# Performance work log

Measured on AMD Instinct MI355X. Metric: run time of the kernel, lower is better.

## Reference

```python
import jax, jax.numpy as jnp
import numpy as np
import math

D_MODEL = 1024
NUM_HEADS = 16
D_HEAD = D_MODEL // NUM_HEADS          # 64
N_FREQ = D_HEAD // 2 + 1               # 33 rfft bins
COMPRESSION_RATIO = 0.5


def setup_inputs() -> dict:
    key = jax.random.key(0)
    k_x, k_qkv, k_out, k_b, k_m = jax.random.split(key, 5)
    B, S = 2, 2048
    x = jax.random.normal(k_x, (B, S, D_MODEL), dtype=jnp.float32)
    # Linear weights stored as [in, out] (torch Linear uses [out, in]; math identical).
    w_qkv = jax.random.normal(k_qkv, (D_MODEL, 3 * D_MODEL), dtype=jnp.float32) / math.sqrt(D_MODEL)
    w_out = jax.random.normal(k_out, (D_MODEL, D_MODEL), dtype=jnp.float32) / math.sqrt(D_MODEL)
    b_out = jax.random.normal(k_b, (D_MODEL,), dtype=jnp.float32) * 0.01
    # Learned per-frequency-bin mask logits of AdaptiveFrequencyMask(d_state=d_head).
    # Initialized around logit(compression_ratio) with small noise.
    init_logit = math.log(COMPRESSION_RATIO / (1.0 - COMPRESSION_RATIO))
    mask_logits = init_logit + 0.1 * jax.random.normal(k_m, (N_FREQ,), dtype=jnp.float32)
    return {"x": x, "w_qkv": w_qkv, "w_out": w_out, "b_out": b_out, "mask_logits": mask_logits}


def _spectral_filter(t, mask):
    # rfft over d_head dim, apply learned soft mask, inverse rfft.  t: [B,H,S,dh]
    tf = jnp.fft.rfft(t, axis=-1)          # [B,H,S,N_FREQ] complex
    tf = tf * mask                          # broadcast real mask over bins
    return jnp.fft.irfft(tf, n=t.shape[-1], axis=-1).astype(t.dtype)


def reference(x, w_qkv, w_out, b_out, mask_logits):
    B, S, D = x.shape
    H, dh = NUM_HEADS, D_HEAD
    qkv = x @ w_qkv                                         # [B,S,3D]
    q, k, v = jnp.split(qkv, 3, axis=-1)
    # [B,S,D] -> [B,H,S,dh]
    to_heads = lambda t: t.reshape(B, S, H, dh).transpose(0, 2, 1, 3)
    q, k, v = to_heads(q), to_heads(k), to_heads(v)
    mask = jax.nn.sigmoid(mask_logits)                      # [N_FREQ]
    q = _spectral_filter(q, mask)
    k = _spectral_filter(k, mask)
    scores = jnp.einsum('bhqd,bhkd->bhqk', q, k) / math.sqrt(dh)
    attn = jax.nn.softmax(scores, axis=-1)                  # dropout p=0 (eval)
    out = jnp.einsum('bhqk,bhkd->bhqd', attn, v)
    out = out.transpose(0, 2, 1, 3).reshape(B, S, D)
    return out @ w_out + b_out
```

## Files before the change

### kernel.cpp

```cpp
#include <hip/hip_runtime.h>

#define S_LEN 2048
#define NH    16
#define DH    64
#define DM    1024
#define NQKV  3072

typedef __attribute__((ext_vector_type(8))) __bf16 bf16x8;
typedef __attribute__((ext_vector_type(4))) float  f32x4;
typedef unsigned short ushort_t;

static __device__ __forceinline__ unsigned short bf16b(float f) {
  return __builtin_bit_cast(unsigned short, (__bf16)f);
}

static __device__ __forceinline__ float exp2v(float x) {
  return __builtin_amdgcn_exp2f(x);
}

static __device__ __forceinline__ bf16x8 pack8(float4 f0, float4 f1) {
  uint4 v;
  v.x = ((unsigned)bf16b(f0.y) << 16) | bf16b(f0.x);
  v.y = ((unsigned)bf16b(f0.w) << 16) | bf16b(f0.z);
  v.z = ((unsigned)bf16b(f1.y) << 16) | bf16b(f1.x);
  v.w = ((unsigned)bf16b(f1.w) << 16) | bf16b(f1.z);
  return __builtin_bit_cast(bf16x8, v);
}

static __device__ __forceinline__ void glds16(const void* g, void* l) {
  __builtin_amdgcn_global_load_lds((const __attribute__((address_space(1))) unsigned int*)g,
                                   (__attribute__((address_space(3))) unsigned int*)l, 16, 0, 0);
}

#define OFF_WT  65536ull
#define OFF_WOT 6356992ull
#define OFF_Q   8454144ull
#define OFF_K   16842752ull
#define OFF_V   25231360ull
#define OFF_AO  33619968ull

__global__ __launch_bounds__(256) void k_prep(const float* __restrict__ wqkv,
                                              const float* __restrict__ wout,
                                              const float* __restrict__ x,
                                              const float* __restrict__ logits,
                                              unsigned short* __restrict__ Wt,
                                              unsigned short* __restrict__ Wot,
                                              unsigned short* __restrict__ xb) {
  __shared__ __align__(16) char sbuf[16640];
  int bid = blockIdx.x;
  int t = threadIdx.x;

  if (bid < 256) {
    float* msk = (float*)sbuf;
    float* Kd  = (float*)(sbuf + 144);
    ushort_t (*Fb)[72] = (ushort_t(*)[72])(sbuf + 416);
    if (t < 33) msk[t] = 1.0f / (1.0f + __expf(-logits[t]));
    __syncthreads();
    if (t < 64) {
      float acc = msk[0];
      #pragma unroll
      for (int f = 1; f < 32; ++f) {
        int r = (f * t) & 63;
        acc += 2.0f * msk[f] * __cosf((float)r * (6.28318530717958647692f / 64.0f));
      }
      acc += msk[32] * ((t & 1) ? -1.0f : 1.0f);
      Kd[t] = acc * (1.0f / 64.0f);
    }
    __syncthreads();
    for (int idx = t; idx < 4096; idx += 256) {
      int j = idx >> 6, i = idx & 63;
      Fb[j][i] = bf16b(Kd[(j - i) & 63]);
    }
    __syncthreads();

    int lane = t & 63, w = t >> 6;
    int m16 = lane & 15, quad = lane >> 4;
    int kx = bid >> 5, yy = bid & 31;
    int which = yy >> 4, h = yy & 15;
    int base = which * 1024 + h * 64;

    bf16x8 af0 = *(const bf16x8*)(&Fb[w * 16 + m16][quad * 8]);
    bf16x8 af1 = *(const bf16x8*)(&Fb[w * 16 + m16][32 + quad * 8]);

    f32x4 acc[8] = {};
    #pragma unroll 2
    for (int n = 0; n < 8; ++n) {
      const float* Wg = wqkv + (size_t)(kx * 128 + n * 16 + m16) * NQKV + base + quad * 8;
      float4 a0 = *(const float4*)(Wg);
      float4 a1 = *(const float4*)(Wg + 4);
      float4 b0 = *(const float4*)(Wg + 32);
      float4 b1 = *(const float4*)(Wg + 36);
      acc[n] = __builtin_amdgcn_mfma_f32_16x16x32_bf16(af0, pack8(a0, a1), acc[n], 0, 0, 0);
      acc[n] = __builtin_amdgcn_mfma_f32_16x16x32_bf16(af1, pack8(b0, b1), acc[n], 0, 0, 0);
    }
    float sc = (which == 0) ? 0.18033688011112042f : 1.0f;
    #pragma unroll
    for (int n = 0; n < 8; ++n) {
      #pragma unroll
      for (int r = 0; r < 4; ++r) {
        int j = w * 16 + quad * 4 + r;
        Wt[(size_t)(base + j) * DM + kx * 128 + n * 16 + m16] = bf16b(acc[n][r] * sc);
      }
    }
  } else if (bid < 768) {
    float (*Ts)[65] = (float(*)[65])sbuf;
    int b1 = bid - 256;
    if (b1 < 256) {
      int kt = b1 & 15, nt = b1 >> 4;
      int cb = 2048 + nt * 64, kbase = kt * 64;
      #pragma unroll
      for (int p = 0; p < 16; ++p) {
        int kk = p * 4 + (t >> 6);
        Ts[kk][t & 63] = wqkv[(size_t)(kbase + kk) * NQKV + cb + (t & 63)];
      }
      __syncthreads();
      #pragma unroll
      for (int p = 0; p < 16; ++p) {
        int nn = p * 4 + (t >> 6);
        Wt[(size_t)(cb + nn) * DM + kbase + (t & 63)] = bf16b(Ts[t & 63][nn]);
      }
    } else {
      int b2 = b1 - 256;
      int kt = b2 & 15, nt = b2 >> 4;
      int cb = nt * 64, kbase = kt * 64;
      #pragma unroll
      for (int p = 0; p < 16; ++p) {
        int kk = p * 4 + (t >> 6);
        Ts[kk][t & 63] = wout[(size_t)(kbase + kk) * DM + cb + (t & 63)];
      }
      __syncthreads();
      #pragma unroll
      for (int p = 0; p < 16; ++p) {
        int nn = p * 4 + (t >> 6);
        Wot[(size_t)(cb + nn) * DM + kbase + (t & 63)] = bf16b(Ts[t & 63][nn]);
      }
    }
  } else {
    size_t i = ((size_t)(bid - 768) * 256 + t) * 8;
    const float4* xp = (const float4*)(x + i);
    float4 a = xp[0], b = xp[1];
    uint4 v;
    v.x = ((unsigned)bf16b(a.y) << 16) | bf16b(a.x);
    v.y = ((unsigned)bf16b(a.w) << 16) | bf16b(a.z);
    v.z = ((unsigned)bf16b(b.y) << 16) | bf16b(b.x);
    v.w = ((unsigned)bf16b(b.w) << 16) | bf16b(b.z);
    *(uint4*)(xb + i) = v;
  }
}

template<int BM, int BN, int WCOLS, int MR, int NR>
__device__ __forceinline__ void gemm_core2(const unsigned short* __restrict__ A,
                                           const unsigned short* __restrict__ Bw,
                                           int bm, int bn, unsigned short* smem,
                                           f32x4 (&acc)[MR][NR]) {
  constexpr int SLOT = (BM + BN) * 64;
  constexpr int PA = BM / 64, PB = BN / 64;
  constexpr int L = PA + PB;
  int t = threadIdx.x, lane = t & 63, w = t >> 6;
  int m16 = lane & 15, quad = lane >> 4;
  int wr = (w / WCOLS) * (MR * 16), wc = (w % WCOLS) * (NR * 16);
  int xr = m16 & 7;
  int trow = t >> 3, tcol = t & 7;
  int gsw = (tcol ^ (trow & 7)) * 8;
  const unsigned short* Ag = A  + (size_t)(bm * BM + trow) * DM + gsw;
  const unsigned short* Bg = Bw + (size_t)(bn * BN + trow) * DM + gsw;
  unsigned short* Al = smem + trow * 64 + tcol * 8;
  unsigned short* Bl = smem + BM * 64 + trow * 64 + tcol * 8;

  #pragma unroll
  for (int s = 0; s < 2; ++s) {
    #pragma unroll
    for (int p = 0; p < PA; ++p)
      glds16(Ag + (size_t)p * 64 * DM + s * 64, Al + s * SLOT + p * 4096);
    #pragma unroll
    for (int p = 0; p < PB; ++p)
      glds16(Bg + (size_t)p * 64 * DM + s * 64, Bl + s * SLOT + p * 4096);
  }

  #pragma unroll 1
  for (int ks = 0; ks < 16; ++ks) {
    if (ks < 15) asm volatile("s_waitcnt vmcnt(%0)" :: "n"(L) : "memory");
    else         asm volatile("s_waitcnt vmcnt(0)" ::: "memory");
    __builtin_amdgcn_s_barrier();
    __builtin_amdgcn_sched_barrier(0);
    const unsigned short* As = smem + (ks & 1) * SLOT;
    const unsigned short* Bs = As + BM * 64;
    #pragma unroll
    for (int kk = 0; kk < 2; ++kk) {
      bf16x8 af[MR], bfr[NR];
      #pragma unroll
      for (int i = 0; i < MR; ++i)
        af[i] = *(const bf16x8*)(As + (wr + i * 16 + m16) * 64 + ((kk * 4 + quad) ^ xr) * 8);
      #pragma unroll
      for (int j = 0; j < NR; ++j)
        bfr[j] = *(const bf16x8*)(Bs + (wc + j * 16 + m16) * 64 + ((kk * 4 + quad) ^ xr) * 8);
      #pragma unroll
      for (int i = 0; i < MR; ++i)
        #pragma unroll
        for (int j = 0; j < NR; ++j)
          acc[i][j] = __builtin_amdgcn_mfma_f32_16x16x32_bf16(af[i], bfr[j], acc[i][j], 0, 0, 0);
    }
    if (ks < 14) {
      __builtin_amdgcn_s_barrier();
      __builtin_amdgcn_sched_barrier(0);
      int kn = ks + 2;
      #pragma unroll
      for (int p = 0; p < PA; ++p)
        glds16(Ag + (size_t)p * 64 * DM + kn * 64, Al + (ks & 1) * SLOT + p * 4096);
      #pragma unroll
      for (int p = 0; p < PB; ++p)
        glds16(Bg + (size_t)p * 64 * DM + kn * 64, Bl + (ks & 1) * SLOT + p * 4096);
    }
  }
  __syncthreads();
}

__global__ __launch_bounds__(512, 1) void k_gemm_qkv(const unsigned short* __restrict__ xb,
                                                     const unsigned short* __restrict__ Bw,
                                                     unsigned short* __restrict__ Qb,
                                                     unsigned short* __restrict__ Kb,
                                                     unsigned short* __restrict__ Vt) {
  __shared__ __align__(16) unsigned short smem[65536];
  f32x4 acc[8][4] = {};
  int bn = blockIdx.x, bm = blockIdx.y;
  gemm_core2<256, 256, 4, 8, 4>(xb, Bw, bm, bn, smem, acc);

  int t = threadIdx.x, lane = t & 63, w = t >> 6;
  int m16 = lane & 15, quad = lane >> 4;
  int b = bm >> 3, srow = (bm & 7) * 256;
  int which = bn >> 2;
  ushort_t (*Tr)[264] = (ushort_t(*)[264])smem;

  if (which < 2) {
    unsigned short* dstB = which ? Kb : Qb;
    int hbase = (bn & 3) * 4;
    #pragma unroll
    for (int ch = 0; ch < 2; ++ch) {
      if ((w >> 2) == ch) {
        #pragma unroll
        for (int i = 0; i < 8; ++i)
          #pragma unroll
          for (int j = 0; j < 4; ++j)
            #pragma unroll
            for (int r = 0; r < 4; ++r)
              Tr[i * 16 + quad * 4 + r][(w & 3) * 64 + j * 16 + m16] = bf16b(acc[i][j][r]);
      }
      __syncthreads();
      int row = t >> 2, qh = t & 3;
      unsigned short* dst = dstB +
          ((size_t)(b * 16 + hbase + qh) * 2048 + srow + ch * 128 + row) * 64;
      #pragma unroll
      for (int p = 0; p < 8; ++p)
        *(uint4*)(dst + p * 8) = *(const uint4*)(&Tr[row][qh * 64 + p * 8]);
      __syncthreads();
    }
  } else {
    int hb = (bn - 8) * 4;
    #pragma unroll
    for (int ch = 0; ch < 2; ++ch) {
      if (((w >> 1) & 1) == ch) {
        #pragma unroll
        for (int i = 0; i < 8; ++i)
          #pragma unroll
          for (int j = 0; j < 4; ++j)
            #pragma unroll
            for (int r = 0; r < 4; ++r)
              Tr[(w & 1) * 64 + j * 16 + m16][(w >> 2) * 128 + i * 16 + quad * 4 + r] =
                  bf16b(acc[i][j][r]);
      }
      __syncthreads();
      int c = t >> 2, qh = t & 3;
      int h = hb + ch * 2 + (c >> 6), d = c & 63;
      unsigned short* dst = Vt + ((size_t)(b * 16 + h) * 64 + d) * 2048 + srow;
      #pragma unroll
      for (int p = 0; p < 8; ++p)
        *(uint4*)(dst + qh * 64 + p * 8) = *(const uint4*)(&Tr[c][qh * 64 + p * 8]);
      __syncthreads();
    }
  }
}

__global__ __launch_bounds__(512, 2) void k_attn(const unsigned short* __restrict__ Qb,
                                                 const unsigned short* __restrict__ Kb,
                                                 const unsigned short* __restrict__ Vt,
                                                 unsigned short* __restrict__ AO) {
  __shared__ __align__(16) unsigned short smem[32768];
  int t = threadIdx.x;
  int w = t >> 6, lane = t & 63;
  int m16 = lane & 15, quad = lane >> 4;
  int bid = blockIdx.x;
  int jj = bid >> 3;
  int bh = ((jj & 3) << 3) + (bid & 7);
  int qbase = (jj >> 2) * 256 + w * 32;

  const unsigned short* QpA = Qb + ((size_t)bh * S_LEN + qbase + m16) * DH + quad * 8;
  const unsigned short* QpB = QpA + 16 * DH;
  bf16x8 aq0A = *(const bf16x8*)(QpA);
  bf16x8 aq1A = *(const bf16x8*)(QpA + 32);
  bf16x8 aq0B = *(const bf16x8*)(QpB);
  bf16x8 aq1B = *(const bf16x8*)(QpB + 32);
  const unsigned short* Kbase = Kb + (size_t)bh * S_LEN * DH;
  const unsigned short* Vbase = Vt + (size_t)bh * DH * S_LEN;

  int xr = m16 & 7;
  int krow0 = ((m16 >> 2) << 3) + (m16 & 3);

  int trow = t >> 3;
  int tcol = t & 7;
  int gswzK = tcol ^ ((trow & 3) | ((trow >> 1) & 4));
  int gswzV = tcol ^ (trow & 7);
  const unsigned short* Kg = Kbase + (size_t)trow * 64 + gswzK * 8;
  const unsigned short* Vg = Vbase + (size_t)trow * S_LEN + gswzV * 8;
  unsigned short* Kl = smem + trow * 64 + tcol * 8;
  unsigned short* Vl = smem + 16384 + trow * 64 + tcol * 8;

  f32x4 oA[4] = {}, oB[4] = {};
  float lA = 0.f, lB = 0.f;
  f32x4 zero = {0.f, 0.f, 0.f, 0.f};

  #pragma unroll
  for (int tt = 0; tt < 4; ++tt) {
    glds16(Kg + (size_t)tt * 4096, Kl + tt * 4096);
    glds16(Vg + tt * 64,           Vl + tt * 4096);
  }

#define QK_TILE(KSH, SA, SB)                                                              \
    _Pragma("unroll")                                                                     \
    for (int c = 0; c < 2; ++c) {                                                         \
      _Pragma("unroll")                                                                   \
      for (int gl = 0; gl < 2; ++gl) {                                                    \
        int key = c * 32 + krow0 + gl * 4;                                                \
        bf16x8 kf0 = *(const bf16x8*)((KSH) + key * 64 + ((quad ^ xr) * 8));              \
        bf16x8 kf1 = *(const bf16x8*)((KSH) + key * 64 + (((4 + quad) ^ xr) * 8));        \
        SA[c][gl] = __builtin_amdgcn_mfma_f32_16x16x32_bf16(kf0, aq0A, zero, 0, 0, 0);    \
        SA[c][gl] = __builtin_amdgcn_mfma_f32_16x16x32_bf16(kf1, aq1A, SA[c][gl], 0, 0, 0);\
        SB[c][gl] = __builtin_amdgcn_mfma_f32_16x16x32_bf16(kf0, aq0B, zero, 0, 0, 0);    \
        SB[c][gl] = __builtin_amdgcn_mfma_f32_16x16x32_bf16(kf1, aq1B, SB[c][gl], 0, 0, 0);\
      }                                                                                   \
    }

#define SM_TILE(SA, SB, PA_, PB_)                                                         \
    _Pragma("unroll")                                                                     \
    for (int c = 0; c < 2; ++c) {                                                         \
      float a0 = exp2v(SA[c][0][0]), a1 = exp2v(SA[c][0][1]);                             \
      float a2 = exp2v(SA[c][0][2]), a3 = exp2v(SA[c][0][3]);                             \
      float a4 = exp2v(SA[c][1][0]), a5 = exp2v(SA[c][1][1]);                             \
      float a6 = exp2v(SA[c][1][2]), a7 = exp2v(SA[c][1][3]);                             \
      lA += ((a0 + a1) + (a2 + a3)) + ((a4 + a5) + (a6 + a7));                            \
      uint4 ua;                                                                           \
      ua.x = ((unsigned)bf16b(a1) << 16) | bf16b(a0);                                     \
      ua.y = ((unsigned)bf16b(a3) << 16) | bf16b(a2);                                     \
      ua.z = ((unsigned)bf16b(a5) << 16) | bf16b(a4);                                     \
      ua.w = ((unsigned)bf16b(a7) << 16) | bf16b(a6);                                     \
      PA_[c] = __builtin_bit_cast(bf16x8, ua);                                            \
      float b0 = exp2v(SB[c][0][0]), b1 = exp2v(SB[c][0][1]);                             \
      float b2 = exp2v(SB[c][0][2]), b3 = exp2v(SB[c][0][3]);                             \
      float b4 = exp2v(SB[c][1][0]), b5 = exp2v(SB[c][1][1]);                             \
      float b6 = exp2v(SB[c][1][2]), b7 = exp2v(SB[c][1][3]);                             \
      lB += ((b0 + b1) + (b2 + b3)) + ((b4 + b5) + (b6 + b7));                            \
      uint4 ub;                                                                           \
      ub.x = ((unsigned)bf16b(b1) << 16) | bf16b(b0);                                     \
      ub.y = ((unsigned)bf16b(b3) << 16) | bf16b(b2);                                     \
      ub.z = ((unsigned)bf16b(b5) << 16) | bf16b(b4);                                     \
      ub.w = ((unsigned)bf16b(b7) << 16) | bf16b(b6);                                     \
      PB_[c] = __builtin_bit_cast(bf16x8, ub);                                            \
    }

#define PV_TILE(VSH, PA_, PB_)                                                            \
    _Pragma("unroll")                                                                     \
    for (int c = 0; c < 2; ++c) {                                                         \
      _Pragma("unroll")                                                                   \
      for (int j = 0; j < 4; ++j) {                                                       \
        int dv = j * 16 + m16;                                                            \
        bf16x8 bv = *(const bf16x8*)((VSH) + dv * 64 + (((c * 4 + quad) ^ xr) * 8));      \
        oA[j] = __builtin_amdgcn_mfma_f32_16x16x32_bf16(PA_[c], bv, oA[j], 0, 0, 0);      \
        oB[j] = __builtin_amdgcn_mfma_f32_16x16x32_bf16(PB_[c], bv, oB[j], 0, 0, 0);      \
      }                                                                                   \
    }

  #pragma unroll 1
  for (int wnd = 0; wnd < 16; ++wnd) {
    if (wnd < 15) asm volatile("s_waitcnt vmcnt(4)" ::: "memory");
    else          asm volatile("s_waitcnt vmcnt(0)" ::: "memory");
    __builtin_amdgcn_s_barrier();
    __builtin_amdgcn_sched_barrier(0);
    int sb = (wnd & 1) << 1;
    const unsigned short* Ka  = smem + sb * 4096;
    const unsigned short* Kbs = smem + (sb + 1) * 4096;
    const unsigned short* Va  = smem + 16384 + sb * 4096;
    const unsigned short* Vbs = smem + 16384 + (sb + 1) * 4096;

    f32x4 sA[2][2], sB[2][2];
    QK_TILE(Ka, sA, sB)
    bf16x8 paA[2], paB[2];
    SM_TILE(sA, sB, paA, paB)
    f32x4 tA[2][2], tB[2][2];
    QK_TILE(Kbs, tA, tB)
    PV_TILE(Va, paA, paB)
    bf16x8 pbA[2], pbB[2];
    SM_TILE(tA, tB, pbA, pbB)
    PV_TILE(Vbs, pbA, pbB)

    if (wnd < 14) {
      __builtin_amdgcn_s_barrier();
      int ta = 2 * wnd + 4;
      glds16(Kg + (size_t)ta * 4096,       Kl + sb * 4096);
      glds16(Vg + ta * 64,                 Vl + sb * 4096);
      glds16(Kg + (size_t)(ta + 1) * 4096, Kl + (sb + 1) * 4096);
      glds16(Vg + (ta + 1) * 64,           Vl + (sb + 1) * 4096);
    }
  }
#undef QK_TILE
#undef SM_TILE
#undef PV_TILE

  lA += __shfl_xor(lA, 16); lA += __shfl_xor(lA, 32);
  lB += __shfl_xor(lB, 16); lB += __shfl_xor(lB, 32);
  float ivA = 1.0f / lA;
  float ivB = 1.0f / lB;
  int b = bh >> 4, h = bh & 15;
  #pragma unroll
  for (int r = 0; r < 4; ++r) {
    float vA = __shfl(ivA, quad * 4 + r);
    float vB = __shfl(ivB, quad * 4 + r);
    size_t row0 = (size_t)b * S_LEN + qbase + quad * 4 + r;
    unsigned short* d0 = AO + row0 * DM + h * DH + m16;
    unsigned short* d1 = AO + (row0 + 16) * DM + h * DH + m16;
    #pragma unroll
    for (int j = 0; j < 4; ++j) {
      d0[j * 16] = bf16b(oA[j][r] * vA);
      d1[j * 16] = bf16b(oB[j][r] * vB);
    }
  }
}

__global__ __launch_bounds__(512, 1) void k_gemm_out(const unsigned short* __restrict__ A,
                                                     const unsigned short* __restrict__ Bw,
                                                     const float* __restrict__ bias,
                                                     float* __restrict__ out) {
  __shared__ __align__(16) unsigned short smem[32768];
  f32x4 acc[4][2] = {};
  int bn = blockIdx.x, bm = blockIdx.y;
  gemm_core2<128, 128, 4, 4, 2>(A, Bw, bm, bn, smem, acc);

  int t = threadIdx.x, lane = t & 63, w = t >> 6;
  int m16 = lane & 15, quad = lane >> 4;
  int wr = (w >> 2) * 64, wc = (w & 3) * 32;
  #pragma unroll
  for (int i = 0; i < 4; ++i) {
    int grow = bm * 128 + wr + i * 16 + quad * 4;
    #pragma unroll
    for (int j = 0; j < 2; ++j) {
      int gc = bn * 128 + wc + j * 16 + m16;
      float bb = bias[gc];
      #pragma unroll
      for (int r = 0; r < 4; ++r)
        out[(size_t)(grow + r) * DM + gc] = acc[i][j][r] + bb;
    }
  }
}

extern "C" void kernel_launch(void* const* d_in, const int* in_sizes, int n_in,
                              void* d_out, int out_size, void* d_ws, size_t ws_size,
                              hipStream_t stream) {
  const float* x    = (const float*)d_in[0];
  const float* wqkv = (const float*)d_in[1];
  const float* wout = (const float*)d_in[2];
  const float* bout = (const float*)d_in[3];
  const float* mlog = (const float*)d_in[4];
  char* ws = (char*)d_ws;
  unsigned short* Wt  = (unsigned short*)(ws + OFF_WT);
  unsigned short* Wot = (unsigned short*)(ws + OFF_WOT);
  unsigned short* Qb  = (unsigned short*)(ws + OFF_Q);
  unsigned short* Kb  = (unsigned short*)(ws + OFF_K);
  unsigned short* Vt  = (unsigned short*)(ws + OFF_V);
  unsigned short* xb  = (unsigned short*)(ws + OFF_AO);
  unsigned short* AO  = (unsigned short*)(ws + OFF_AO);
  float* out = (float*)d_out;

  k_prep<<<dim3(2816), dim3(256), 0, stream>>>(wqkv, wout, x, mlog, Wt, Wot, xb);
  k_gemm_qkv<<<dim3(12, 16), dim3(512), 0, stream>>>(xb, Wt, Qb, Kb, Vt);
  k_attn<<<dim3(256), dim3(512), 0, stream>>>(Qb, Kb, Vt, AO);
  k_gemm_out<<<dim3(8, 32), dim3(512), 0, stream>>>(AO, Wot, bout, out);
}
```

Measured before the change: 185.0 us.

## Retile QKV GEMM to 256x192 and deepen attention K/V prefetch ring

```diff
diff --git a/kernel.cpp b/kernel.cpp
--- a/kernel.cpp
+++ b/kernel.cpp
@@ -220,62 +220,47 @@
                                                      unsigned short* __restrict__ Qb,
                                                      unsigned short* __restrict__ Kb,
                                                      unsigned short* __restrict__ Vt) {
-  __shared__ __align__(16) unsigned short smem[65536];
-  f32x4 acc[8][4] = {};
+  __shared__ __align__(16) unsigned short smem[57344];
+  f32x4 acc[8][3] = {};
   int bn = blockIdx.x, bm = blockIdx.y;
-  gemm_core2<256, 256, 4, 8, 4>(xb, Bw, bm, bn, smem, acc);
+  gemm_core2<256, 192, 4, 8, 3>(xb, Bw, bm, bn, smem, acc);
 
   int t = threadIdx.x, lane = t & 63, w = t >> 6;
   int m16 = lane & 15, quad = lane >> 4;
+  int wr = (w >> 2) * 128, wc = (w & 3) * 48;
   int b = bm >> 3, srow = (bm & 7) * 256;
-  int which = bn >> 2;
-  ushort_t (*Tr)[264] = (ushort_t(*)[264])smem;
-
-  if (which < 2) {
-    unsigned short* dstB = which ? Kb : Qb;
-    int hbase = (bn & 3) * 4;
-    #pragma unroll
-    for (int ch = 0; ch < 2; ++ch) {
-      if ((w >> 2) == ch) {
+  ushort_t (*Tr)[200] = (ushort_t(*)[200])smem;
+
+  #pragma unroll
+  for (int i = 0; i < 8; ++i)
+    #pragma unroll
+    for (int j = 0; j < 3; ++j)
+      #pragma unroll
+      for (int r = 0; r < 4; ++r)
+        Tr[wr + i * 16 + quad * 4 + r][wc + j * 16 + m16] = bf16b(acc[i][j][r]);
+  __syncthreads();
+
+  #pragma unroll
+  for (int ch = 0; ch < 3; ++ch) {
+    int cb = bn * 192 + ch * 64;
+    int which = cb >> 10, hcol = (cb >> 6) & 15;
+    if (which < 2) {
+      int row = t >> 1, part = t & 1;
+      unsigned short* dst = (which ? Kb : Qb) +
+          ((size_t)(b * 16 + hcol) * 2048 + srow + row) * 64 + part * 32;
+      #pragma unroll
+      for (int p = 0; p < 4; ++p)
+        *(uint4*)(dst + p * 8) = *(const uint4*)(&Tr[row][ch * 64 + part * 32 + p * 8]);
+    } else {
+      int d = t & 63, rb = (t >> 6) * 32;
+      unsigned short* dst = Vt + ((size_t)(b * 16 + hcol) * 64 + d) * 2048 + srow + rb;
+      #pragma unroll
+      for (int p = 0; p < 4; ++p) {
+        unsigned short tmp[8];
         #pragma unroll
-        for (int i = 0; i < 8; ++i)
-          #pragma unroll
-          for (int j = 0; j < 4; ++j)
-            #pragma unroll
-            for (int r = 0; r < 4; ++r)
-              Tr[i * 16 + quad * 4 + r][(w & 3) * 64 + j * 16 + m16] = bf16b(acc[i][j][r]);
-      }
-      __syncthreads();
-      int row = t >> 2, qh = t & 3;
-      unsigned short* dst = dstB +
-          ((size_t)(b * 16 + hbase + qh) * 2048 + srow + ch * 128 + row) * 64;
-      #pragma unroll
-      for (int p = 0; p < 8; ++p)
-        *(uint4*)(dst + p * 8) = *(const uint4*)(&Tr[row][qh * 64 + p * 8]);
-      __syncthreads();
-    }
-  } else {
-    int hb = (bn - 8) * 4;
-    #pragma unroll
-    for (int ch = 0; ch < 2; ++ch) {
-      if (((w >> 1) & 1) == ch) {
-        #pragma unroll
-        for (int i = 0; i < 8; ++i)
-          #pragma unroll
-          for (int j = 0; j < 4; ++j)
-            #pragma unroll
-            for (int r = 0; r < 4; ++r)
-              Tr[(w & 1) * 64 + j * 16 + m16][(w >> 2) * 128 + i * 16 + quad * 4 + r] =
-                  bf16b(acc[i][j][r]);
-      }
-      __syncthreads();
-      int c = t >> 2, qh = t & 3;
-      int h = hb + ch * 2 + (c >> 6), d = c & 63;
-      unsigned short* dst = Vt + ((size_t)(b * 16 + h) * 64 + d) * 2048 + srow;
-      #pragma unroll
-      for (int p = 0; p < 8; ++p)
-        *(uint4*)(dst + qh * 64 + p * 8) = *(const uint4*)(&Tr[c][qh * 64 + p * 8]);
-      __syncthreads();
+        for (int q = 0; q < 8; ++q) tmp[q] = Tr[rb + p * 8 + q][ch * 64 + d];
+        *(uint4*)(dst + p * 8) = *(const uint4*)tmp;
+      }
     }
   }
 }
@@ -284,7 +269,7 @@
                                                  const unsigned short* __restrict__ Kb,
                                                  const unsigned short* __restrict__ Vt,
                                                  unsigned short* __restrict__ AO) {
-  __shared__ __align__(16) unsigned short smem[32768];
+  __shared__ __align__(16) unsigned short smem[65536];
   int t = threadIdx.x;
   int w = t >> 6, lane = t & 63;
   int m16 = lane & 15, quad = lane >> 4;
@@ -312,14 +297,14 @@
   const unsigned short* Kg = Kbase + (size_t)trow * 64 + gswzK * 8;
   const unsigned short* Vg = Vbase + (size_t)trow * S_LEN + gswzV * 8;
   unsigned short* Kl = smem + trow * 64 + tcol * 8;
-  unsigned short* Vl = smem + 16384 + trow * 64 + tcol * 8;
+  unsigned short* Vl = smem + 32768 + trow * 64 + tcol * 8;
 
   f32x4 oA[4] = {}, oB[4] = {};
   float lA = 0.f, lB = 0.f;
   f32x4 zero = {0.f, 0.f, 0.f, 0.f};
 
   #pragma unroll
-  for (int tt = 0; tt < 4; ++tt) {
+  for (int tt = 0; tt < 6; ++tt) {
     glds16(Kg + (size_t)tt * 4096, Kl + tt * 4096);
     glds16(Vg + tt * 64,           Vl + tt * 4096);
   }
@@ -380,35 +365,40 @@
 
   #pragma unroll 1
   for (int wnd = 0; wnd < 16; ++wnd) {
-    if (wnd < 15) asm volatile("s_waitcnt vmcnt(4)" ::: "memory");
-    else          asm volatile("s_waitcnt vmcnt(0)" ::: "memory");
+    if (wnd < 14)      asm volatile("s_waitcnt vmcnt(8)" ::: "memory");
+    else if (wnd < 15) asm volatile("s_waitcnt vmcnt(4)" ::: "memory");
+    else               asm volatile("s_waitcnt vmcnt(0)" ::: "memory");
     __builtin_amdgcn_s_barrier();
     __builtin_amdgcn_sched_barrier(0);
-    int sb = (wnd & 1) << 1;
-    const unsigned short* Ka  = smem + sb * 4096;
-    const unsigned short* Kbs = smem + (sb + 1) * 4096;
-    const unsigned short* Va  = smem + 16384 + sb * 4096;
-    const unsigned short* Vbs = smem + 16384 + (sb + 1) * 4096;
+    if (wnd < 13) {
+      int ta = 2 * wnd + 6;
+      glds16(Kg + (size_t)ta * 4096,       Kl + (ta & 7) * 4096);
+      glds16(Vg + ta * 64,                 Vl + (ta & 7) * 4096);
+      glds16(Kg + (size_t)(ta + 1) * 4096, Kl + ((ta + 1) & 7) * 4096);
+      glds16(Vg + (ta + 1) * 64,           Vl + ((ta + 1) & 7) * 4096);
+    }
+    int s0 = (2 * wnd) & 7, s1 = (2 * wnd + 1) & 7;
+    const unsigned short* Ka  = smem + s0 * 4096;
+    const unsigned short* Kbs = smem + s1 * 4096;
+    const unsigned short* Va  = smem + 32768 + s0 * 4096;
+    const unsigned short* Vbs = smem + 32768 + s1 * 4096;
 
     f32x4 sA[2][2], sB[2][2];
+    __builtin_amdgcn_s_setprio(1);
     QK_TILE(Ka, sA, sB)
+    __builtin_amdgcn_s_setprio(0);
     bf16x8 paA[2], paB[2];
     SM_TILE(sA, sB, paA, paB)
     f32x4 tA[2][2], tB[2][2];
+    __builtin_amdgcn_s_setprio(1);
     QK_TILE(Kbs, tA, tB)
     PV_TILE(Va, paA, paB)
+    __builtin_amdgcn_s_setprio(0);
     bf16x8 pbA[2], pbB[2];
     SM_TILE(tA, tB, pbA, pbB)
+    __builtin_amdgcn_s_setprio(1);
     PV_TILE(Vbs, pbA, pbB)
-
-    if (wnd < 14) {
-      __builtin_amdgcn_s_barrier();
-      int ta = 2 * wnd + 4;
-      glds16(Kg + (size_t)ta * 4096,       Kl + sb * 4096);
-      glds16(Vg + ta * 64,                 Vl + sb * 4096);
-      glds16(Kg + (size_t)(ta + 1) * 4096, Kl + (sb + 1) * 4096);
-      glds16(Vg + (ta + 1) * 64,           Vl + (sb + 1) * 4096);
-    }
+    __builtin_amdgcn_s_setprio(0);
   }
 #undef QK_TILE
 #undef SM_TILE
@@ -479,7 +469,7 @@
   float* out = (float*)d_out;
 
   k_prep<<<dim3(2816), dim3(256), 0, stream>>>(wqkv, wout, x, mlog, Wt, Wot, xb);
-  k_gemm_qkv<<<dim3(12, 16), dim3(512), 0, stream>>>(xb, Wt, Qb, Kb, Vt);
+  k_gemm_qkv<<<dim3(16, 16), dim3(512), 0, stream>>>(xb, Wt, Qb, Kb, Vt);
   k_attn<<<dim3(256), dim3(512), 0, stream>>>(Qb, Kb, Vt, AO);
   k_gemm_out<<<dim3(8, 32), dim3(512), 0, stream>>>(AO, Wot, bout, out);
 }
```

After: 185.6 us. Within noise of the previous version (+0.3%).

## Deepen attention K/V ring buffer, add setprio, remap QKV GEMM blocks per XCD

Applied to the files above, without the earlier changes.

```diff
diff --git a/kernel.cpp b/kernel.cpp
--- a/kernel.cpp
+++ b/kernel.cpp
@@ -222,7 +222,10 @@
                                                      unsigned short* __restrict__ Vt) {
   __shared__ __align__(16) unsigned short smem[65536];
   f32x4 acc[8][4] = {};
-  int bn = blockIdx.x, bm = blockIdx.y;
+  int bid = blockIdx.x;
+  int xcd = bid & 7, loc = bid >> 3;
+  int bm = xcd * 2 + (loc / 12);
+  int bn = loc % 12;
   gemm_core2<256, 256, 4, 8, 4>(xb, Bw, bm, bn, smem, acc);
 
   int t = threadIdx.x, lane = t & 63, w = t >> 6;
@@ -284,7 +287,7 @@
                                                  const unsigned short* __restrict__ Kb,
                                                  const unsigned short* __restrict__ Vt,
                                                  unsigned short* __restrict__ AO) {
-  __shared__ __align__(16) unsigned short smem[32768];
+  __shared__ __align__(16) unsigned short smem[65536];
   int t = threadIdx.x;
   int w = t >> 6, lane = t & 63;
   int m16 = lane & 15, quad = lane >> 4;
@@ -312,14 +315,14 @@
   const unsigned short* Kg = Kbase + (size_t)trow * 64 + gswzK * 8;
   const unsigned short* Vg = Vbase + (size_t)trow * S_LEN + gswzV * 8;
   unsigned short* Kl = smem + trow * 64 + tcol * 8;
-  unsigned short* Vl = smem + 16384 + trow * 64 + tcol * 8;
+  unsigned short* Vl = smem + 32768 + trow * 64 + tcol * 8;
 
   f32x4 oA[4] = {}, oB[4] = {};
   float lA = 0.f, lB = 0.f;
   f32x4 zero = {0.f, 0.f, 0.f, 0.f};
 
   #pragma unroll
-  for (int tt = 0; tt < 4; ++tt) {
+  for (int tt = 0; tt < 6; ++tt) {
     glds16(Kg + (size_t)tt * 4096, Kl + tt * 4096);
     glds16(Vg + tt * 64,           Vl + tt * 4096);
   }
@@ -380,35 +383,40 @@
 
   #pragma unroll 1
   for (int wnd = 0; wnd < 16; ++wnd) {
-    if (wnd < 15) asm volatile("s_waitcnt vmcnt(4)" ::: "memory");
-    else          asm volatile("s_waitcnt vmcnt(0)" ::: "memory");
+    if (wnd < 14)      asm volatile("s_waitcnt vmcnt(8)" ::: "memory");
+    else if (wnd < 15) asm volatile("s_waitcnt vmcnt(4)" ::: "memory");
+    else               asm volatile("s_waitcnt vmcnt(0)" ::: "memory");
     __builtin_amdgcn_s_barrier();
     __builtin_amdgcn_sched_barrier(0);
-    int sb = (wnd & 1) << 1;
-    const unsigned short* Ka  = smem + sb * 4096;
-    const unsigned short* Kbs = smem + (sb + 1) * 4096;
-    const unsigned short* Va  = smem + 16384 + sb * 4096;
-    const unsigned short* Vbs = smem + 16384 + (sb + 1) * 4096;
+    if (wnd < 13) {
+      int ta = 2 * wnd + 6;
+      glds16(Kg + (size_t)ta * 4096,       Kl + (ta & 7) * 4096);
+      glds16(Vg + ta * 64,                 Vl + (ta & 7) * 4096);
+      glds16(Kg + (size_t)(ta + 1) * 4096, Kl + ((ta + 1) & 7) * 4096);
+      glds16(Vg + (ta + 1) * 64,           Vl + ((ta + 1) & 7) * 4096);
+    }
+    int s0 = (2 * wnd) & 7, s1 = (2 * wnd + 1) & 7;
+    const unsigned short* Ka  = smem + s0 * 4096;
+    const unsigned short* Kbs = smem + s1 * 4096;
+    const unsigned short* Va  = smem + 32768 + s0 * 4096;
+    const unsigned short* Vbs = smem + 32768 + s1 * 4096;
 
     f32x4 sA[2][2], sB[2][2];
+    __builtin_amdgcn_s_setprio(1);
     QK_TILE(Ka, sA, sB)
+    __builtin_amdgcn_s_setprio(0);
     bf16x8 paA[2], paB[2];
     SM_TILE(sA, sB, paA, paB)
     f32x4 tA[2][2], tB[2][2];
+    __builtin_amdgcn_s_setprio(1);
     QK_TILE(Kbs, tA, tB)
     PV_TILE(Va, paA, paB)
+    __builtin_amdgcn_s_setprio(0);
     bf16x8 pbA[2], pbB[2];
     SM_TILE(tA, tB, pbA, pbB)
+    __builtin_amdgcn_s_setprio(1);
     PV_TILE(Vbs, pbA, pbB)
-
-    if (wnd < 14) {
-      __builtin_amdgcn_s_barrier();
-      int ta = 2 * wnd + 4;
-      glds16(Kg + (size_t)ta * 4096,       Kl + sb * 4096);
-      glds16(Vg + ta * 64,                 Vl + sb * 4096);
-      glds16(Kg + (size_t)(ta + 1) * 4096, Kl + (sb + 1) * 4096);
-      glds16(Vg + (ta + 1) * 64,           Vl + (sb + 1) * 4096);
-    }
+    __builtin_amdgcn_s_setprio(0);
   }
 #undef QK_TILE
 #undef SM_TILE
@@ -479,7 +487,7 @@
   float* out = (float*)d_out;
 
   k_prep<<<dim3(2816), dim3(256), 0, stream>>>(wqkv, wout, x, mlog, Wt, Wot, xb);
-  k_gemm_qkv<<<dim3(12, 16), dim3(512), 0, stream>>>(xb, Wt, Qb, Kb, Vt);
+  k_gemm_qkv<<<dim3(192), dim3(512), 0, stream>>>(xb, Wt, Qb, Kb, Vt);
   k_attn<<<dim3(256), dim3(512), 0, stream>>>(Qb, Kb, Vt, AO);
   k_gemm_out<<<dim3(8, 32), dim3(512), 0, stream>>>(AO, Wot, bout, out);
 }
```

New measurement: 182.8 us. About the same (-1.2%).
